# Optimization experiments

Hardware: AMD Instinct MI355X
Metric: run time of the kernel (lower is better)

## Reference

```python
import jax, jax.numpy as jnp
import numpy as np

K = 16        # neighbors
M = 4         # repeat count
EPS = 1e-5    # BatchNorm eps (torch default)


def setup_inputs() -> dict:
    key = jax.random.key(0)
    k1, k2, k3, k4 = jax.random.split(key, 4)
    B, N, C, Fe = 8, 8192, 64, 32  # Fe = int(channels * dim_expand)
    return {
        "xyz": jax.random.normal(k1, (B, N, 3), dtype=jnp.float32),
        "feat": jax.random.normal(k2, (B, C, N), dtype=jnp.float32),
        "bn_gamma": jnp.ones((C,), jnp.float32),
        "bn_beta": jnp.zeros((C,), jnp.float32),
        "Wg": jax.random.normal(k3, (Fe, C + 3), jnp.float32) * 0.1,   # g_func weight [out, in]
        "Wh": jax.random.normal(k4, (C, M * Fe), jnp.float32) * 0.1,   # h_func weight [out, in]
    }


def reference(xyz, feat, bn_gamma, bn_beta, Wg, Wh):
    # xyz: [B, N, 3], feat: [B, C, N]
    # --- bn0: training-mode BatchNorm1d over channel dim (stats over B, N) ---
    mean = feat.mean(axis=(0, 2), keepdims=True)
    var = feat.var(axis=(0, 2), keepdims=True)
    fbn = bn_gamma[None, :, None] * (feat - mean) * jax.lax.rsqrt(var + EPS) + bn_beta[None, :, None]

    # --- g_func on concat(feat_bn, xyz^T) -> feat0 [B, N, Fe] ---
    cat = jnp.concatenate([fbn, jnp.transpose(xyz, (0, 2, 1))], axis=1)  # [B, C+3, N]
    feat0 = jnp.einsum('bcn,ec->bne', cat, Wg)                           # [B, N, Fe]

    # --- bknn: pairwise squared distances, top-k of -dist (computed once) ---
    xx = jnp.sum(xyz * xyz, axis=-1)                                     # [B, N]
    dist = xx[:, :, None] - 2.0 * jnp.einsum('bnd,bmd->bnm', xyz, xyz) + xx[:, None, :]
    _, idx = jax.lax.top_k(-dist, K)                                     # [B, N, K] int32

    # --- gather neighbor features, max-pool over K ---
    group = jax.vmap(lambda f, i: f[i])(feat0, idx)                      # [B, N, K, Fe]
    gmax = group.max(axis=2)                                             # [B, N, Fe]
    rel = gmax - feat0                                                   # [B, N, Fe]

    # Original loop reuses cached idx and feat0 every iteration, so all M
    # concatenated blocks are identical -> tile along the feature dim.
    rel_rep = jnp.concatenate([rel] * M, axis=-1)                        # [B, N, M*Fe]

    # --- h_func -> output [B, C, N] ---
    out = jnp.einsum('bnf,cf->bcn', rel_rep, Wh)
    return out
```

## Files before the change

### kernel.cpp

```cpp
#include <hip/hip_runtime.h>
#include <math.h>

#define BB 8
#define NN 8192
#define CC 64
#define FE 32
#define KN 16
#define CP3 67
#define QPW 4
#define WPB 4
#define CAPQ 64
#define YB 32
#define ZB 32
#define NCELL (YB * ZB)

__device__ double g_part[BB * CC * 2];
__device__ float g_feat0[BB * NN * FE];
__device__ int   g_idx[BB * NN * KN];
__device__ float4 g_sorted[BB * NN];
__device__ int    g_sorig[BB * NN];
__device__ unsigned g_binoff[BB * (NCELL + 1)];

__device__ __forceinline__ int cbin(float v) {
    int bi = (int)((v + 4.5f) * (32.0f / 9.0f));
    if (bi < 0) bi = 0;
    if (bi > 31) bi = 31;
    return bi;
}
__device__ __forceinline__ float frz_xx(float x, float y, float z) {
    return __fmaf_rn(z, z, __fmaf_rn(y, y, __fmul_rn(x, x)));
}

__global__ __launch_bounds__(256) void k_bnstats(const float* __restrict__ feat) {
    int bc = blockIdx.x;
    const float* p = feat + (size_t)bc * NN;
    int tid = threadIdx.x;
    double s = 0.0, s2 = 0.0;
    for (int n = tid; n < NN; n += 256) {
        double v = (double)p[n];
        s += v; s2 += v * v;
    }
    __shared__ double sh[256], sh2[256];
    sh[tid] = s; sh2[tid] = s2;
    __syncthreads();
    for (int off = 128; off > 0; off >>= 1) {
        if (tid < off) { sh[tid] += sh[tid + off]; sh2[tid] += sh2[tid + off]; }
        __syncthreads();
    }
    if (tid == 0) {
        g_part[bc * 2]     = sh[0];
        g_part[bc * 2 + 1] = sh2[0];
    }
}

__global__ __launch_bounds__(1024) void k_zbin(const float* __restrict__ xyz) {
    __shared__ unsigned hist[NCELL];
    __shared__ unsigned scan[NCELL];
    __shared__ unsigned boff[NCELL + 1];
    int b = blockIdx.x;
    int tid = threadIdx.x;
    hist[tid] = 0;
    __syncthreads();
    const float* bx = xyz + (size_t)b * NN * 3;
    for (int n = tid; n < NN; n += 1024) {
        float y = bx[n * 3 + 1], z = bx[n * 3 + 2];
        atomicAdd(&hist[cbin(y) * ZB + cbin(z)], 1u);
    }
    __syncthreads();
    scan[tid] = hist[tid];
    __syncthreads();
    for (int off = 1; off < NCELL; off <<= 1) {
        unsigned add = (tid >= off) ? scan[tid - off] : 0u;
        __syncthreads();
        scan[tid] += add;
        __syncthreads();
    }
    if (tid == 0) boff[0] = 0;
    boff[tid + 1] = scan[tid];
    __syncthreads();
    hist[tid] = 0;
    g_binoff[b * (NCELL + 1) + tid + 1] = boff[tid + 1];
    if (tid == 0) g_binoff[b * (NCELL + 1)] = 0;
    __syncthreads();
    for (int n = tid; n < NN; n += 1024) {
        const float* p = bx + (size_t)n * 3;
        float x = p[0], y = p[1], z = p[2];
        int cell = cbin(y) * ZB + cbin(z);
        unsigned pos = boff[cell] + atomicAdd(&hist[cell], 1u);
        g_sorted[(size_t)b * NN + pos] = make_float4(x, y, z, frz_xx(x, y, z));
        g_sorig[(size_t)b * NN + pos] = n;
    }
}

__global__ __launch_bounds__(256) void k_feat0(const float* __restrict__ feat,
        const float* __restrict__ xyz, const float* __restrict__ Wg,
        const float* __restrict__ gamma, const float* __restrict__ beta) {
    __shared__ float scs[CC], shs[CC];
    __shared__ float wgs[CP3 * FE];
    __shared__ float bias0[FE];
    int tid = threadIdx.x;
    if (tid < CC) {
        double s = 0.0, s2 = 0.0;
        for (int bb2 = 0; bb2 < BB; ++bb2) {
            s  += g_part[((bb2 << 6) + tid) * 2];
            s2 += g_part[((bb2 << 6) + tid) * 2 + 1];
        }
        double inv = 1.0 / (double)(BB * NN);
        double mean = s * inv;
        double var = s2 * inv - mean * mean;
        float sc = gamma[tid] * (float)(1.0 / sqrt(var + (double)1e-5f));
        scs[tid] = sc;
        shs[tid] = beta[tid] - sc * (float)mean;
    }
    __syncthreads();
    for (int i = tid; i < CP3 * FE; i += 256) {
        int c = i >> 5, e = i & 31;
        float w = Wg[e * CP3 + c];
        if (c < CC) w *= scs[c];
        wgs[c * FE + e] = w;
    }
    if (tid < FE) {
        float sacc = 0.f;
        for (int c = 0; c < CC; ++c) sacc = fmaf(Wg[tid * CP3 + c], shs[c], sacc);
        bias0[tid] = sacc;
    }
    __syncthreads();
    int pid = blockIdx.x * 128 + (tid >> 1);
    int half = tid & 1;
    int b = pid >> 13;
    int n = pid & (NN - 1);
    const float* pz = xyz + ((size_t)(b * NN + n)) * 3;
    float x = pz[0], y = pz[1], z = pz[2];

    float acc[16];
    #pragma unroll
    for (int e = 0; e < 16; ++e) acc[e] = bias0[half * 16 + e];
    const float* fp = feat + (size_t)b * CC * NN + n;
    for (int c = 0; c < CC; ++c) {
        float v = fp[(size_t)c * NN];
        const float4* w4 = (const float4*)(wgs + c * FE) + half * 4;
        #pragma unroll
        for (int e0 = 0; e0 < 4; ++e0) {
            float4 w = w4[e0];
            acc[e0 * 4 + 0] = fmaf(w.x, v, acc[e0 * 4 + 0]);
            acc[e0 * 4 + 1] = fmaf(w.y, v, acc[e0 * 4 + 1]);
            acc[e0 * 4 + 2] = fmaf(w.z, v, acc[e0 * 4 + 2]);
            acc[e0 * 4 + 3] = fmaf(w.w, v, acc[e0 * 4 + 3]);
        }
    }
    #pragma unroll
    for (int d = 0; d < 3; ++d) {
        float v = (d == 0) ? x : ((d == 1) ? y : z);
        const float4* w4 = (const float4*)(wgs + (CC + d) * FE) + half * 4;
        #pragma unroll
        for (int e0 = 0; e0 < 4; ++e0) {
            float4 w = w4[e0];
            acc[e0 * 4 + 0] = fmaf(w.x, v, acc[e0 * 4 + 0]);
            acc[e0 * 4 + 1] = fmaf(w.y, v, acc[e0 * 4 + 1]);
            acc[e0 * 4 + 2] = fmaf(w.z, v, acc[e0 * 4 + 2]);
            acc[e0 * 4 + 3] = fmaf(w.w, v, acc[e0 * 4 + 3]);
        }
    }
    float4* outp = ((float4*)(g_feat0 + ((size_t)(b * NN + n)) * FE)) + half * 4;
    #pragma unroll
    for (int e0 = 0; e0 < 4; ++e0)
        outp[e0] = make_float4(acc[e0 * 4 + 0], acc[e0 * 4 + 1], acc[e0 * 4 + 2], acc[e0 * 4 + 3]);
}

__global__ __launch_bounds__(256) void k_knn() {
    __shared__ unsigned long long qbuf[WPB * CAPQ];
    int tid = threadIdx.x;
    int lane = tid & 63;
    int w = tid >> 6;
    int wid = blockIdx.x * WPB + w;
    int b = wid >> 11;
    int g = wid & 2047;
    const float4* S = g_sorted + (size_t)b * NN;
    const int* SO = g_sorig + (size_t)b * NN;
    const unsigned* BO = g_binoff + b * (NCELL + 1);
    unsigned long long lt = (1ull << lane) - 1ull;
    unsigned long long* pb = qbuf + w * CAPQ;

    #pragma unroll 1
    for (int i = 0; i < QPW; ++i) {
        int qrank = g + (i << 11);
        float4 qv = S[qrank];
        float qx = qv.x, qy = qv.y, qz = qv.z, qxx = qv.w;
        int qorig = SO[qrank];
        float tt = 0.053f * __expf(qxx * (1.0f / 3.0f));
        float t0 = tt > 3.f ? 3.f : tt;
        float tlo = 0.f, thi = 0.f;
        unsigned cnt = 0;

        for (int attempt = 0; attempt < 40; ++attempt) {
            cnt = 0;
            float tpe = t0 + 1e-3f;
            float R = __fsqrt_rn(tpe) + 1e-3f;
            int ylo = cbin(qy - R), yhi = cbin(qy + R);

            int yb = ylo, p = 0, hi = 0;
            {
                float rowlo = 0.28125f * (float)yb - 4.5f;
                float dy = fmaxf(0.f, fmaxf(rowlo - qy, qy - (rowlo + 0.28125f)));
                float rz2 = tpe - dy * dy;
                if (rz2 > 0.f) {
                    float Rz = __fsqrt_rn(rz2) + 1e-3f;
                    int zl = cbin(qz - Rz), zh = cbin(qz + Rz);
                    p = (int)BO[yb * ZB + zl]; hi = (int)BO[yb * ZB + zh + 1];
                }
            }
            while (p >= hi && yb < yhi) {
                ++yb;
                float rowlo = 0.28125f * (float)yb - 4.5f;
                float dy = fmaxf(0.f, fmaxf(rowlo - qy, qy - (rowlo + 0.28125f)));
                float rz2 = tpe - dy * dy;
                if (rz2 > 0.f) {
                    float Rz = __fsqrt_rn(rz2) + 1e-3f;
                    int zl = cbin(qz - Rz), zh = cbin(qz + Rz);
                    p = (int)BO[yb * ZB + zl]; hi = (int)BO[yb * ZB + zh + 1];
                } else { p = 0; hi = 0; }
            }
            bool have = p < hi;
            int jc0 = 0, jc1 = 0; bool in0 = false, in1 = false;
            float4 c0, c1;
            if (have) {
                int base = p + 2 * lane;
                jc0 = base < hi ? base : hi - 1;
                jc1 = base + 1 < hi ? base + 1 : hi - 1;
                c0 = S[jc0]; c1 = S[jc1];
                in0 = base < hi; in1 = base + 1 < hi;
            }
            while (have) {
                int yb2 = yb, p2 = p + 128, hi2 = hi;
                while (p2 >= hi2 && yb2 < yhi) {
                    ++yb2;
                    float rowlo = 0.28125f * (float)yb2 - 4.5f;
                    float dy = fmaxf(0.f, fmaxf(rowlo - qy, qy - (rowlo + 0.28125f)));
                    float rz2 = tpe - dy * dy;
                    if (rz2 > 0.f) {
                        float Rz = __fsqrt_rn(rz2) + 1e-3f;
                        int zl = cbin(qz - Rz), zh = cbin(qz + Rz);
                        p2 = (int)BO[yb2 * ZB + zl]; hi2 = (int)BO[yb2 * ZB + zh + 1];
                    } else { p2 = 0; hi2 = 0; }
                }
                bool have2 = p2 < hi2;
                int jn0 = jc0, jn1 = jc1; bool inn0 = false, inn1 = false;
                float4 n0 = c0, n1 = c1;
                if (have2) {
                    int base = p2 + 2 * lane;
                    jn0 = base < hi2 ? base : hi2 - 1;
                    jn1 = base + 1 < hi2 ? base + 1 : hi2 - 1;
                    n0 = S[jn0]; n1 = S[jn1];
                    inn0 = base < hi2; inn1 = base + 1 < hi2;
                }
                float dot0 = __fmaf_rn(qz, c0.z, __fmaf_rn(qy, c0.y, __fmul_rn(qx, c0.x)));
                float dist0 = __fadd_rn(__fmaf_rn(-2.f, dot0, qxx), c0.w);
                float dot1 = __fmaf_rn(qz, c1.z, __fmaf_rn(qy, c1.y, __fmul_rn(qx, c1.x)));
                float dist1 = __fadd_rn(__fmaf_rn(-2.f, dot1, qxx), c1.w);
                bool pr0 = (dist0 <= t0) && in0;
                bool pr1 = (dist1 <= t0) && in1;
                unsigned long long m0 = __ballot(pr0);
                unsigned long long m1 = __ballot(pr1);
                if (m0 | m1) {
                    unsigned n0c = (unsigned)__popcll(m0);
                    unsigned pos0 = cnt + (unsigned)__popcll(m0 & lt);
                    unsigned pos1 = cnt + n0c + (unsigned)__popcll(m1 & lt);
                    if (pr0 && pos0 < CAPQ) {
                        int corig = SO[jc0];
                        int db = __float_as_int(dist0);
                        unsigned key = (unsigned)db ^ (unsigned)((db >> 31) | 0x80000000);
                        pb[pos0] = ((unsigned long long)key << 32) | (unsigned)corig;
                    }
                    if (pr1 && pos1 < CAPQ) {
                        int corig = SO[jc1];
                        int db = __float_as_int(dist1);
                        unsigned key = (unsigned)db ^ (unsigned)((db >> 31) | 0x80000000);
                        pb[pos1] = ((unsigned long long)key << 32) | (unsigned)corig;
                    }
                    cnt += n0c + (unsigned)__popcll(m1);
                }
                yb = yb2; p = p2; hi = hi2; have = have2;
                jc0 = jn0; jc1 = jn1; c0 = n0; c1 = n1; in0 = inn0; in1 = inn1;
            }
            if (cnt < KN) {
                tlo = t0;
                t0 = (thi > 0.f) ? __fsqrt_rn(tlo * thi) : t0 * 2.0f;
            } else if (cnt > CAPQ) {
                thi = t0;
                t0 = (tlo > 0.f) ? __fsqrt_rn(tlo * thi) : t0 * 0.5f;
            } else break;
        }

        unsigned tot = cnt > CAPQ ? CAPQ : cnt;
        unsigned long long e0 = ((unsigned)lane < tot) ? pb[lane] : ~0ull;
        unsigned rank0 = 0;
        for (unsigned jx = 0; jx < tot; ++jx) {
            unsigned long long v = pb[jx];
            rank0 += (v < e0) ? 1u : 0u;
        }
        if (((unsigned)lane < tot) && rank0 < KN)
            g_idx[(b * NN + qorig) * KN + rank0] = (int)(e0 & 0xffffffffull);
    }
}

__global__ __launch_bounds__(256) void k_out(const float* __restrict__ Wh,
        float* __restrict__ out) {
    __shared__ float whs[CC * FE];
    __shared__ float pmax[64][4][33];
    int tid = threadIdx.x;
    for (int i = tid; i < CC * FE; i += 256) {
        int c = i >> 5, e = i & 31;
        float s = 0.f;
        #pragma unroll
        for (int m = 0; m < 4; ++m) s += Wh[c * 128 + m * 32 + e];
        whs[i] = s;
    }
    int pt = tid >> 2, part = tid & 3;
    int pid = blockIdx.x * 64 + pt;
    int b = pid >> 13;
    int n = pid & (NN - 1);
    const int* ip = g_idx + (size_t)(b * NN + n) * KN + part * 4;
    const float4* f0 = (const float4*)(g_feat0 + (size_t)b * NN * FE);
    float gm[FE];
    #pragma unroll
    for (int e = 0; e < FE; ++e) gm[e] = -__builtin_inff();
    #pragma unroll
    for (int k = 0; k < 4; ++k) {
        int id = ip[k] & (NN - 1);
        const float4* row = f0 + (size_t)id * 8;
        #pragma unroll
        for (int e0 = 0; e0 < 8; ++e0) {
            float4 v = row[e0];
            gm[e0 * 4 + 0] = fmaxf(gm[e0 * 4 + 0], v.x);
            gm[e0 * 4 + 1] = fmaxf(gm[e0 * 4 + 1], v.y);
            gm[e0 * 4 + 2] = fmaxf(gm[e0 * 4 + 2], v.z);
            gm[e0 * 4 + 3] = fmaxf(gm[e0 * 4 + 3], v.w);
        }
    }
    #pragma unroll
    for (int e = 0; e < FE; ++e) pmax[pt][part][e] = gm[e];
    __syncthreads();

    const float4* selfr = f0 + (size_t)n * 8;
    float rel[FE];
    #pragma unroll
    for (int e0 = 0; e0 < 8; ++e0) {
        float4 v = selfr[e0];
        #pragma unroll
        for (int j = 0; j < 4; ++j) {
            int e = e0 * 4 + j;
            float gg = fmaxf(fmaxf(pmax[pt][0][e], pmax[pt][1][e]),
                             fmaxf(pmax[pt][2][e], pmax[pt][3][e]));
            float sv = (j == 0) ? v.x : (j == 1) ? v.y : (j == 2) ? v.z : v.w;
            rel[e] = gg - sv;
        }
    }
    float* op = out + (size_t)b * CC * NN + n;
    for (int c = part * 16; c < part * 16 + 16; ++c) {
        const float4* w4 = (const float4*)(whs + c * FE);
        float s = 0.f;
        #pragma unroll
        for (int e0 = 0; e0 < 8; ++e0) {
            float4 w = w4[e0];
            s = fmaf(w.x, rel[e0 * 4 + 0], s);
            s = fmaf(w.y, rel[e0 * 4 + 1], s);
            s = fmaf(w.z, rel[e0 * 4 + 2], s);
            s = fmaf(w.w, rel[e0 * 4 + 3], s);
        }
        op[(size_t)c * NN] = s;
    }
}

extern "C" void kernel_launch(void* const* d_in, const int* in_sizes, int n_in,
                              void* d_out, int out_size, void* d_ws, size_t ws_size,
                              hipStream_t stream) {
    const float* xyz   = (const float*)d_in[0];
    const float* feat  = (const float*)d_in[1];
    const float* gamma = (const float*)d_in[2];
    const float* beta  = (const float*)d_in[3];
    const float* Wg    = (const float*)d_in[4];
    const float* Wh    = (const float*)d_in[5];
    float* out = (float*)d_out;
    (void)d_ws; (void)ws_size;

    hipLaunchKernelGGL(k_bnstats, dim3(512),  dim3(256),  0, stream, feat);
    hipLaunchKernelGGL(k_zbin,    dim3(8),    dim3(1024), 0, stream, xyz);
    hipLaunchKernelGGL(k_feat0,   dim3(512),  dim3(256),  0, stream, feat, xyz, Wg, gamma, beta);
    hipLaunchKernelGGL(k_knn,     dim3(4096), dim3(256),  0, stream);
    hipLaunchKernelGGL(k_out,     dim3(1024), dim3(256),  0, stream, Wh, out);
}
```

Baseline: 190.4 us.

## Split spatial binning into parallel histogram, scan, scatter kernels; tune initial radius

Replaces the single 8-block binning kernel with three kernels: per-slice histograms over 64 blocks, a per-batch prefix scan, and a 64-block scatter that uses per-slice offsets. This spreads the counting-sort work across more of the GPU instead of leaving it on 8 blocks. It also lowers the initial kNN search radius coefficient, which should cut candidate counts but may trigger more retry attempts. The cost is two extra kernel launches and a global partial-histogram buffer.

```diff
diff --git a/kernel.cpp b/kernel.cpp
--- a/kernel.cpp
+++ b/kernel.cpp
@@ -13,6 +13,7 @@
 #define YB 32
 #define ZB 32
 #define NCELL (YB * ZB)
+#define NSL 8
 
 __device__ double g_part[BB * CC * 2];
 __device__ float g_feat0[BB * NN * FE];
@@ -20,6 +21,7 @@
 __device__ float4 g_sorted[BB * NN];
 __device__ int    g_sorig[BB * NN];
 __device__ unsigned g_binoff[BB * (NCELL + 1)];
+__device__ unsigned g_parthist[BB * NSL * NCELL];
 
 __device__ __forceinline__ int cbin(float v) {
     int bi = (int)((v + 4.5f) * (32.0f / 9.0f));
@@ -53,21 +55,29 @@
     }
 }
 
-__global__ __launch_bounds__(1024) void k_zbin(const float* __restrict__ xyz) {
+__global__ __launch_bounds__(1024) void k_hist(const float* __restrict__ xyz) {
     __shared__ unsigned hist[NCELL];
+    int blk = blockIdx.x;
+    int b = blk >> 3, si = blk & 7;
+    int tid = threadIdx.x;
+    hist[tid] = 0;
+    __syncthreads();
+    int n = si * 1024 + tid;
+    const float* p = xyz + ((size_t)(b * NN + n)) * 3;
+    atomicAdd(&hist[cbin(p[1]) * ZB + cbin(p[2])], 1u);
+    __syncthreads();
+    g_parthist[(size_t)(b * NSL + si) * NCELL + tid] = hist[tid];
+}
+
+__global__ __launch_bounds__(1024) void k_scan() {
     __shared__ unsigned scan[NCELL];
-    __shared__ unsigned boff[NCELL + 1];
     int b = blockIdx.x;
     int tid = threadIdx.x;
-    hist[tid] = 0;
-    __syncthreads();
-    const float* bx = xyz + (size_t)b * NN * 3;
-    for (int n = tid; n < NN; n += 1024) {
-        float y = bx[n * 3 + 1], z = bx[n * 3 + 2];
-        atomicAdd(&hist[cbin(y) * ZB + cbin(z)], 1u);
-    }
-    __syncthreads();
-    scan[tid] = hist[tid];
+    unsigned s = 0;
+    #pragma unroll
+    for (int si = 0; si < NSL; ++si)
+        s += g_parthist[(size_t)(b * NSL + si) * NCELL + tid];
+    scan[tid] = s;
     __syncthreads();
     for (int off = 1; off < NCELL; off <<= 1) {
         unsigned add = (tid >= off) ? scan[tid - off] : 0u;
@@ -75,21 +85,27 @@
         scan[tid] += add;
         __syncthreads();
     }
-    if (tid == 0) boff[0] = 0;
-    boff[tid + 1] = scan[tid];
-    __syncthreads();
-    hist[tid] = 0;
-    g_binoff[b * (NCELL + 1) + tid + 1] = boff[tid + 1];
+    g_binoff[b * (NCELL + 1) + tid + 1] = scan[tid];
     if (tid == 0) g_binoff[b * (NCELL + 1)] = 0;
-    __syncthreads();
-    for (int n = tid; n < NN; n += 1024) {
-        const float* p = bx + (size_t)n * 3;
-        float x = p[0], y = p[1], z = p[2];
-        int cell = cbin(y) * ZB + cbin(z);
-        unsigned pos = boff[cell] + atomicAdd(&hist[cell], 1u);
-        g_sorted[(size_t)b * NN + pos] = make_float4(x, y, z, frz_xx(x, y, z));
-        g_sorig[(size_t)b * NN + pos] = n;
-    }
+}
+
+__global__ __launch_bounds__(1024) void k_scatter(const float* __restrict__ xyz) {
+    __shared__ unsigned cur[NCELL];
+    int blk = blockIdx.x;
+    int b = blk >> 3, si = blk & 7;
+    int tid = threadIdx.x;
+    unsigned base = g_binoff[b * (NCELL + 1) + tid];
+    for (int s2 = 0; s2 < si; ++s2)
+        base += g_parthist[(size_t)(b * NSL + s2) * NCELL + tid];
+    cur[tid] = base;
+    __syncthreads();
+    int n = si * 1024 + tid;
+    const float* p = xyz + ((size_t)(b * NN + n)) * 3;
+    float x = p[0], y = p[1], z = p[2];
+    int cell = cbin(y) * ZB + cbin(z);
+    unsigned pos = atomicAdd(&cur[cell], 1u);
+    g_sorted[(size_t)b * NN + pos] = make_float4(x, y, z, frz_xx(x, y, z));
+    g_sorig[(size_t)b * NN + pos] = n;
 }
 
 __global__ __launch_bounds__(256) void k_feat0(const float* __restrict__ feat,
@@ -187,7 +203,7 @@
         float4 qv = S[qrank];
         float qx = qv.x, qy = qv.y, qz = qv.z, qxx = qv.w;
         int qorig = SO[qrank];
-        float tt = 0.053f * __expf(qxx * (1.0f / 3.0f));
+        float tt = 0.045f * __expf(qxx * (1.0f / 3.0f));
         float t0 = tt > 3.f ? 3.f : tt;
         float tlo = 0.f, thi = 0.f;
         unsigned cnt = 0;
@@ -384,7 +400,9 @@
     (void)d_ws; (void)ws_size;
 
     hipLaunchKernelGGL(k_bnstats, dim3(512),  dim3(256),  0, stream, feat);
-    hipLaunchKernelGGL(k_zbin,    dim3(8),    dim3(1024), 0, stream, xyz);
+    hipLaunchKernelGGL(k_hist,    dim3(64),   dim3(1024), 0, stream, xyz);
+    hipLaunchKernelGGL(k_scan,    dim3(8),    dim3(1024), 0, stream);
+    hipLaunchKernelGGL(k_scatter, dim3(64),   dim3(1024), 0, stream, xyz);
     hipLaunchKernelGGL(k_feat0,   dim3(512),  dim3(256),  0, stream, feat, xyz, Wg, gamma, beta);
     hipLaunchKernelGGL(k_knn,     dim3(4096), dim3(256),  0, stream);
     hipLaunchKernelGGL(k_out,     dim3(1024), dim3(256),  0, stream, Wh, out);
```

Measured after the change: 178.9 us. -6.1%, faster.
